# Kernel optimization log

Measured on AMD Instinct MI355X. Metric: run time of the kernel, lower is better.

Reference implementation:

```python
import jax, jax.numpy as jnp
import numpy as np

B, S, N, D = 4, 12, 716, 64
H = 4            # num_heads
ALPHA = 0.2      # LeakyReLU negative slope
NEG = -9e15      # mask fill value from the torch code (-9000000000000000.0)


def setup_inputs() -> dict:
    key = jax.random.key(0)
    ks = jax.random.split(key, 20)
    sc = 1.0 / np.sqrt(D)
    inputs = jax.random.normal(ks[0], (B, S, N, D), dtype=jnp.float32)
    adj = jax.random.randint(ks[1], (N, N), 0, 2).astype(jnp.int32)
    in_degree = jax.random.randint(ks[2], (N,), 0, N)
    out_degree = jax.random.randint(ks[3], (N,), 0, N)
    # embeddings with padding_idx=0 -> row 0 zeroed
    in_emb = (jax.random.normal(ks[4], (N, D)) * sc).at[0].set(0.0)
    out_emb = (jax.random.normal(ks[5], (N, D)) * sc).at[0].set(0.0)
    # GAT params
    W = jax.random.normal(ks[6], (D, D)) * sc
    a1 = jax.random.normal(ks[7], (D, 1)) * sc
    a2 = jax.random.normal(ks[8], (D, 1)) * sc
    # spatial multi-head attention params
    Wq = jax.random.normal(ks[9], (D, D)) * sc
    bq = jnp.zeros((D,))
    Wk = jax.random.normal(ks[10], (D, D)) * sc
    bk = jnp.zeros((D,))
    Wv = jax.random.normal(ks[11], (D, D)) * sc
    bv = jnp.zeros((D,))
    Wo = jax.random.normal(ks[12], (D, D)) * sc
    bo = jnp.zeros((D,))
    # pred_linear: 2D -> D
    Wp = jax.random.normal(ks[13], (2 * D, D)) * (1.0 / np.sqrt(2 * D))
    bp = jnp.zeros((D,))
    return dict(inputs=inputs, adj=adj, in_degree=in_degree, out_degree=out_degree,
                in_emb=in_emb, out_emb=out_emb, W=W, a1=a1, a2=a2,
                Wq=Wq, bq=bq, Wk=Wk, bk=bk, Wv=Wv, bv=bv, Wo=Wo, bo=bo,
                Wp=Wp, bp=bp)


def reference(inputs, adj, in_degree, out_degree, in_emb, out_emb,
              W, a1, a2, Wq, bq, Wk, bk, Wv, bv, Wo, bo, Wp, bp):
    b, s, n, d = inputs.shape
    dh = d // H
    # degree embeddings, broadcast over batch & time: [N, D]
    spatial_emb = in_emb[in_degree] + out_emb[out_degree]

    # ---- GAT, vectorized over all batch*seq samples (orig loops per sample) ----
    x = inputs.reshape(b * s, n, d)
    Wh = jnp.einsum('bnd,de->bne', x, W)                 # [BS, N, D]
    Wh1 = Wh @ a1                                        # [BS, N, 1]
    Wh2 = Wh @ a2                                        # [BS, N, 1]
    e = Wh1 + jnp.swapaxes(Wh2, 1, 2)                    # [BS, N, N]
    e = jnp.where(e > 0, e, ALPHA * e)                   # LeakyReLU
    e = jnp.where(adj[None] > 0, e, NEG)                 # adjacency mask
    attn = jax.nn.softmax(e, axis=-1)                    # softmax(dim=1) on 2D == last axis
    out1 = jax.nn.elu(attn @ Wh).reshape(b, s, n, d)     # dropout is identity in eval

    # ---- Spatial multi-head attention over nodes ----
    y = inputs + spatial_emb                             # [B, S, N, D]
    q = (y @ Wq + bq).reshape(b, s, n, H, dh)
    k = (y @ Wk + bk).reshape(b, s, n, H, dh)
    v = (y @ Wv + bv).reshape(b, s, n, H, dh)
    scores = jnp.einsum('bsnhk,bsmhk->bshnm', q, k) / jnp.sqrt(jnp.float32(dh))
    p = jax.nn.softmax(scores, axis=-1)                  # [B, S, H, N, N]
    o = jnp.einsum('bshnm,bsmhk->bsnhk', p, v).reshape(b, s, n, d)
    out2 = o @ Wo + bo

    # ---- fuse and project ----
    return jnp.concatenate([out1, out2], axis=-1) @ Wp + bp
```

## Files before the change

kernel.cpp:

```cpp
#include <hip/hip_runtime.h>
#include <hip/hip_bf16.h>

#define BN   716
#define BD   64
#define BH   4
#define BDH  16
#define BBS  48
#define NCH  23
#define NJT  45
#define QSCALE 0.3606737602f

typedef __hip_bfloat16 bf16;
typedef __attribute__((ext_vector_type(8))) short short8;
typedef __attribute__((ext_vector_type(4))) short s16x4;
typedef __attribute__((ext_vector_type(4))) float f32x4;

__device__ __forceinline__ float b2f(bf16 x){ return __bfloat162float(x); }
__device__ __forceinline__ bf16 f2b(float x){ return __float2bfloat16(x); }
__device__ __forceinline__ short bfbits(float x){
  union { bf16 h; short s; } c; c.h = __float2bfloat16(x); return c.s;
}
__device__ __forceinline__ unsigned packbf(float a, float b){
  unsigned ua = __float_as_uint(a) + 0x8000u;
  unsigned ub = __float_as_uint(b) + 0x8000u;
  return __builtin_amdgcn_perm(ub, ua, 0x07060302u);
}
__device__ __forceinline__ short8 pack8(float a,float b,float c,float d,
                                        float e,float f,float g,float h){
  short8 r; r[0]=bfbits(a); r[1]=bfbits(b); r[2]=bfbits(c); r[3]=bfbits(d);
  r[4]=bfbits(e); r[5]=bfbits(f); r[6]=bfbits(g); r[7]=bfbits(h); return r;
}
__device__ __forceinline__ float fexp2(float x){
#if __has_builtin(__builtin_amdgcn_exp2f)
  return __builtin_amdgcn_exp2f(x);
#else
  return __expf(x * 0.6931471805599453f);
#endif
}
__device__ __forceinline__ float frcp(float x){
#if __has_builtin(__builtin_amdgcn_rcpf)
  return __builtin_amdgcn_rcpf(x);
#else
  return 1.0f / x;
#endif
}

#define MFMA16(a,b,c) __builtin_amdgcn_mfma_f32_16x16x32_bf16(a,b,c,0,0,0)

#if __has_builtin(__builtin_amdgcn_mfma_f32_16x16x16_bf16)
#define HAVE_MFMA16K 1
__device__ __forceinline__ f32x4 mfma16k(s16x4 a, s16x4 b, f32x4 c){
  return __builtin_amdgcn_mfma_f32_16x16x16_bf16(a, b, c, 0, 0, 0);
}
#elif __has_builtin(__builtin_amdgcn_mfma_f32_16x16x16bf16_1k)
#define HAVE_MFMA16K 1
__device__ __forceinline__ f32x4 mfma16k(s16x4 a, s16x4 b, f32x4 c){
  return __builtin_amdgcn_mfma_f32_16x16x16bf16_1k(a, b, c, 0, 0, 0);
}
#else
#define HAVE_MFMA16K 0
#endif

__global__ __launch_bounds__(256) void k_prep(
    const int* __restrict__ adj,
    const float* __restrict__ W,  const float* __restrict__ Wq,
    const float* __restrict__ Wk, const float* __restrict__ Wv,
    const float* __restrict__ Wo, const float* __restrict__ bo,
    const float* __restrict__ Wp, const float* __restrict__ bp,
    unsigned* __restrict__ mask, bf16* __restrict__ WB,
    bf16* __restrict__ WF, float* __restrict__ bfuse)
{
  int b = blockIdx.x, t = threadIdx.x;
  if (b < 65){
    int w = b * 256 + t;
    if (w < BN * NCH){
      int row = w / NCH, wc = w - row * NCH;
      unsigned m = 0;
      int jb = wc * 32;
      for (int bb = 0; bb < 32; bb++){
        int j = jb + bb;
        if (j < BN && adj[(long)row * BN + j] > 0) m |= (1u << bb);
      }
      mask[w] = m;
    }
  } else if (b < 69){
#pragma unroll
    for (int i = 0; i < 16; i++){
      int idx = (b - 65) * 4096 + i * 256 + t;
      int n = idx >> 6, kk = idx & 63;
      const float* src = (n < 64) ? W : (n < 128) ? Wq : (n < 192) ? Wk : Wv;
      WB[idx] = f2b(src[kk * BD + (n & 63)]);
    }
  } else if (b < 101){
    int idx = (b - 69) * 256 + t;
    int n = idx >> 7, kk = idx & 127;
    float v;
    if (kk < 64){
      v = Wp[kk * BD + n];
    } else {
      v = 0.f;
      int r = kk - 64;
      for (int m = 0; m < BD; m++)
        v += Wo[r * BD + m] * Wp[(BD + m) * BD + n];
    }
    WF[idx] = f2b(v);
  } else {
    if (t < BD){
      float acc = bp[t];
      for (int m = 0; m < BD; m++)
        acc += bo[m] * Wp[(BD + m) * BD + t];
      bfuse[t] = acc;
    }
  }
}

__global__ __launch_bounds__(256) void k_proj(
    const float* __restrict__ x,
    const int* __restrict__ ind, const int* __restrict__ outd,
    const float* __restrict__ in_emb, const float* __restrict__ out_emb,
    const float* __restrict__ a1p, const float* __restrict__ a2p,
    const bf16* __restrict__ WB,
    const float* __restrict__ bq, const float* __restrict__ bk, const float* __restrict__ bv,
    bf16* __restrict__ WhS, float* __restrict__ Wh1, float2* __restrict__ EwP,
    bf16* __restrict__ Qt, bf16* __restrict__ Kt, bf16* __restrict__ Vt16)
{
  __shared__ short stA[64][72];
  __shared__ short stB[64][72];
  __shared__ short stC[64][72];
  __shared__ short stD[64][72];
  int bs = blockIdx.x, tile = blockIdx.y;
  int n0 = tile * 64;
  int t = threadIdx.x, w = t >> 6, lane = t & 63, quad = lane >> 4, l15 = lane & 15;
  long sb = (long)bs * BN;
  int rowi = n0 + w * 16 + l15;
  int rc = rowi < BN ? rowi : BN - 1;
  const float* xr  = x + (sb + rc) * BD;
  const float* ier = in_emb  + (long)ind [rc] * BD;
  const float* oer = out_emb + (long)outd[rc] * BD;

  f32x4 aw[4], aqkv[12];
#pragma unroll
  for (int i2 = 0; i2 < 4;  i2++) aw[i2]   = (f32x4){0,0,0,0};
#pragma unroll
  for (int i2 = 0; i2 < 12; i2++) aqkv[i2] = (f32x4){0,0,0,0};

#pragma unroll
  for (int kc = 0; kc < 2; kc++){
    int k0 = kc * 32 + quad * 8;
    float4 xa = *(const float4*)(xr  + k0);
    float4 xb = *(const float4*)(xr  + k0 + 4);
    float4 ia = *(const float4*)(ier + k0);
    float4 ib = *(const float4*)(ier + k0 + 4);
    float4 oa = *(const float4*)(oer + k0);
    float4 ob = *(const float4*)(oer + k0 + 4);
    short8 ax = pack8(xa.x, xa.y, xa.z, xa.w, xb.x, xb.y, xb.z, xb.w);
    short8 ay = pack8(xa.x+ia.x+oa.x, xa.y+ia.y+oa.y, xa.z+ia.z+oa.z, xa.w+ia.w+oa.w,
                      xb.x+ib.x+ob.x, xb.y+ib.y+ob.y, xb.z+ib.z+ob.z, xb.w+ib.w+ob.w);
#pragma unroll
    for (int nt = 0; nt < 4; nt++)
      aw[nt] = MFMA16(ax, *(const short8*)(WB + (nt*16 + l15) * BD + k0), aw[nt]);
#pragma unroll
    for (int nt = 0; nt < 12; nt++)
      aqkv[nt] = MFMA16(ay, *(const short8*)(WB + (64 + nt*16 + l15) * BD + k0), aqkv[nt]);
  }

  {
    float s1v[4] = {0,0,0,0}, s2v[4] = {0,0,0,0};
#pragma unroll
    for (int nt = 0; nt < 4; nt++){
      float a1f = a1p[nt*16 + l15], a2f = a2p[nt*16 + l15];
#pragma unroll
      for (int reg = 0; reg < 4; reg++){
        s1v[reg] += aw[nt][reg] * a1f;
        s2v[reg] += aw[nt][reg] * a2f;
      }
    }
#pragma unroll
    for (int off = 1; off < 16; off <<= 1){
#pragma unroll
      for (int reg = 0; reg < 4; reg++){
        s1v[reg] += __shfl_xor(s1v[reg], off);
        s2v[reg] += __shfl_xor(s2v[reg], off);
      }
    }
    if (l15 == 0){
#pragma unroll
      for (int reg = 0; reg < 4; reg++){
        int rr = n0 + w*16 + quad*4 + reg;
        if (rr < BN){
          Wh1[sb + rr] = s1v[reg];
          float s2 = s2v[reg];
          EwP[sb + rr] = make_float2(__expf(s2), __expf(0.2f * s2));
        }
      }
    }
  }

#pragma unroll
  for (int nt = 0; nt < 4; nt++){
    *(short4*)&stA[nt*16 + l15][w*16 + quad*4] = make_short4(
        bfbits(aw[nt][0]), bfbits(aw[nt][1]), bfbits(aw[nt][2]), bfbits(aw[nt][3]));
    float bb = bv[nt*16 + l15];
    *(short4*)&stB[nt*16 + l15][w*16 + quad*4] = make_short4(
        bfbits(aqkv[8+nt][0]+bb), bfbits(aqkv[8+nt][1]+bb),
        bfbits(aqkv[8+nt][2]+bb), bfbits(aqkv[8+nt][3]+bb));
    float bq_ = bq[nt*16 + l15];
    float bk_ = bk[nt*16 + l15];
#pragma unroll
    for (int reg = 0; reg < 4; reg++){
      stC[w*16 + quad*4 + reg][nt*16 + l15] = bfbits((aqkv[nt][reg] + bq_) * QSCALE);
      stD[w*16 + quad*4 + reg][nt*16 + l15] = bfbits(aqkv[4+nt][reg] + bk_);
    }
  }
  __syncthreads();

#pragma unroll
  for (int s = 0; s < 2; s++){
    int L = (t*2 + s) * 8;
    int kb = L & 31, d = (L >> 5) & 63, chl = L >> 11;
    int ch = tile * 2 + chl;
    if (ch < NCH)
      *(uint4*)(WhS + (((long)bs*NCH + ch)*64 + d)*32 + kb) = *(const uint4*)&stA[d][chl*32 + kb];
  }
  {
    int jl = t >> 6;
    int c  = t & 15, qq = (t >> 4) & 3;
    int jt = tile * 4 + jl;
    if (jt < NJT){
#pragma unroll
      for (int h = 0; h < BH; h++){
        s16x4 v4 = *(const s16x4*)&stB[h*16 + c][jl*16 + qq*4];
        *(s16x4*)(Vt16 + ((((long)bs*BH + h)*NJT + jt)*64 + (t & 63))*4) = v4;
      }
    }
  }
#pragma unroll
  for (int s = 0; s < 2; s++){
    int L = (t*2 + s) * 8;
    int kb = L & 15, nl = (L >> 4) & 63, h = L >> 10;
    int jt = tile * 4 + (nl >> 4);
    if (jt < NJT){
      *(uint4*)(Qt + ((((long)bs*BH + h)*NJT + jt)*16 + (nl&15))*16 + kb)
          = *(const uint4*)&stC[nl][h*16 + kb];
      *(uint4*)(Kt + ((((long)bs*BH + h)*NJT + jt)*16 + (nl&15))*16 + kb)
          = *(const uint4*)&stD[nl][h*16 + kb];
    }
  }
}

__global__ __launch_bounds__(256) void k_attn(
    const float* __restrict__ Wh1, const float2* __restrict__ EwP,
    const unsigned* __restrict__ mask, const bf16* __restrict__ WhS,
    const bf16* __restrict__ Qt, const bf16* __restrict__ Kt,
    const bf16* __restrict__ Vt16,
    bf16* __restrict__ out1, bf16* __restrict__ o)
{
#if !HAVE_MFMA16K
  __shared__ short pw[4][16][48];
#endif
  int bs = blockIdx.x, yb = blockIdx.y;
  int t = threadIdx.x, w = t >> 6, lane = t & 63, quad = lane >> 4, l15 = lane & 15;
  long sb = (long)bs * BN;

  if (yb < 12){
    int rt = yb * 4 + w;
    if (rt >= NJT) return;
    int i = rt * 16 + l15;
    int ic = i < BN ? i : BN - 1;
    float e1 = Wh1[sb + ic];
    float Aa = __expf(e1), Cc = __expf(0.2f * e1);
    float invA = frcp(Aa);
    const unsigned* mrow = mask + (long)ic * NCH;
    const float2* ew = EwP + sb;

    float sl = 0.f;
    f32x4 acc0 = {0,0,0,0}, acc1 = {0,0,0,0}, acc2 = {0,0,0,0}, acc3 = {0,0,0,0};
    for (int ch = 0; ch < NCH; ch++){
      int j0 = ch * 32 + quad * 8;
      unsigned m8 = (mrow[ch] >> (quad * 8)) & 0xFFu;
      const float4* ef = (const float4*)(ew + j0);
      float4 q0 = ef[0], q1 = ef[1], q2 = ef[2], q3 = ef[3];
      float Bv[8] = {q0.x, q0.z, q1.x, q1.z, q2.x, q2.z, q3.x, q3.z};
      float Dv[8] = {q0.y, q0.w, q1.y, q1.w, q2.y, q2.w, q3.y, q3.w};
      float p[8];
#pragma unroll
      for (int jj = 0; jj < 8; jj++){
        bool cond = Bv[jj] > invA;
        float f = cond ? Bv[jj] : Dv[jj];
        float g = cond ? Aa : Cc;
        float pp = ((m8 >> jj) & 1u) ? f * g : 0.f;
        sl += pp;
        p[jj] = pp;
      }
      union { unsigned u[4]; short8 v; } A;
      A.u[0] = packbf(p[0], p[1]); A.u[1] = packbf(p[2], p[3]);
      A.u[2] = packbf(p[4], p[5]); A.u[3] = packbf(p[6], p[7]);
      const bf16* wbp = WhS + ((long)bs*NCH + ch)*2048 + quad * 8;
      acc0 = MFMA16(A.v, *(const short8*)(wbp + ( 0 + l15) * 32), acc0);
      acc1 = MFMA16(A.v, *(const short8*)(wbp + (16 + l15) * 32), acc1);
      acc2 = MFMA16(A.v, *(const short8*)(wbp + (32 + l15) * 32), acc2);
      acc3 = MFMA16(A.v, *(const short8*)(wbp + (48 + l15) * 32), acc3);
    }
    sl += __shfl_xor(sl, 16);
    sl += __shfl_xor(sl, 32);
    float inv[4];
#pragma unroll
    for (int reg = 0; reg < 4; reg++){
      int srcl = quad * 4 + reg;
      float s = __int_as_float(__builtin_amdgcn_ds_bpermute(srcl << 2, __float_as_int(sl)));
      inv[reg] = 1.0f / s;
    }
    const f32x4* accs[4] = {&acc0, &acc1, &acc2, &acc3};
#pragma unroll
    for (int nt = 0; nt < 4; nt++){
#pragma unroll
      for (int reg = 0; reg < 4; reg++){
        int gi = rt * 16 + quad * 4 + reg;
        if (gi < BN){
          float val = (*accs[nt])[reg] * inv[reg];
          val = (val > 0.f) ? val : (__expf(val) - 1.f);
          out1[(sb + gi) * BD + nt*16 + l15] = f2b(val);
        }
      }
    }
    return;
  }

  int h = w, rt = yb - 12;
  const bf16* Qh = Qt   + ((long)bs*BH + h) * NJT * 256;
  const bf16* Kh = Kt   + ((long)bs*BH + h) * NJT * 256;
  const bf16* Vh = Vt16 + ((long)bs*BH + h) * NJT * 256;

  f32x4 oacc = {0,0,0,0};
  float psum = 0.f;

#if HAVE_MFMA16K
  s16x4 bq16 = *(const s16x4*)(Qh + rt*256 + l15*16 + quad*4);
#pragma unroll 4
  for (int jt = 0; jt < NJT - 1; jt++){
    s16x4 ak = *(const s16x4*)(Kh + jt*256 + l15*16 + quad*4);
    f32x4 c = mfma16k(ak, bq16, ((f32x4){0,0,0,0}));
    float p[4];
#pragma unroll
    for (int reg = 0; reg < 4; reg++){
      float pp = fexp2(c[reg]);
      psum += pp;
      p[reg] = pp;
    }
    union { unsigned u[2]; s16x4 v; } A;
    A.u[0] = packbf(p[0], p[1]); A.u[1] = packbf(p[2], p[3]);
    s16x4 bv = *(const s16x4*)(Vh + jt*256 + lane*4);
    oacc = mfma16k(A.v, bv, oacc);
  }
  {
    int jt = NJT - 1;
    s16x4 ak = *(const s16x4*)(Kh + jt*256 + l15*16 + quad*4);
    f32x4 c = mfma16k(ak, bq16, ((f32x4){0,0,0,0}));
    float p[4];
#pragma unroll
    for (int reg = 0; reg < 4; reg++){
      float pp = (quad == 3) ? 0.f : fexp2(c[reg]);
      psum += pp;
      p[reg] = pp;
    }
    union { unsigned u[2]; s16x4 v; } A;
    A.u[0] = packbf(p[0], p[1]); A.u[1] = packbf(p[2], p[3]);
    s16x4 bv = *(const s16x4*)(Vh + jt*256 + lane*4);
    oacc = mfma16k(A.v, bv, oacc);
  }
#else
  short8 aq = {0,0,0,0,0,0,0,0};
  if (quad < 2) aq = *(const short8*)(Qh + rt*256 + l15*16 + quad*8);
  for (int ch = 0; ch < NCH; ch++){
#pragma unroll
    for (int tt = 0; tt < 2; tt++){
      int jt = 2*ch + tt;
      if (jt < NJT){
        short8 ak = {0,0,0,0,0,0,0,0};
        if (quad < 2) ak = *(const short8*)(Kh + jt*256 + l15*16 + quad*8);
        f32x4 c = MFMA16(ak, aq, ((f32x4){0,0,0,0}));
        bool inval = (jt == NJT-1) && (quad == 3);
#pragma unroll
        for (int reg = 0; reg < 4; reg++){
          float pp = fexp2(c[reg]);
          pp = inval ? 0.f : pp;
          psum += pp;
          pw[h][l15][tt*16 + quad*4 + reg] = (short)((__float_as_uint(pp) + 0x8000u) >> 16);
        }
      } else {
#pragma unroll
        for (int reg = 0; reg < 4; reg++) pw[h][l15][tt*16 + quad*4 + reg] = 0;
      }
    }
    short8 ap = *(const short8*)&pw[h][l15][quad*8];
    int jB = 2*ch + (quad >> 1);
    s16x4 v0 = {0,0,0,0}, v1 = {0,0,0,0};
    if (jB < NJT){
      v0 = *(const s16x4*)(Vh + jB*256 + (((quad&1)*2  )*16 + l15)*4);
      v1 = *(const s16x4*)(Vh + jB*256 + (((quad&1)*2+1)*16 + l15)*4);
    }
    short8 bv8; bv8[0]=v0[0]; bv8[1]=v0[1]; bv8[2]=v0[2]; bv8[3]=v0[3];
    bv8[4]=v1[0]; bv8[5]=v1[1]; bv8[6]=v1[2]; bv8[7]=v1[3];
    oacc = MFMA16(ap, bv8, oacc);
  }
#endif

  psum += __shfl_xor(psum, 16);
  psum += __shfl_xor(psum, 32);
#pragma unroll
  for (int reg = 0; reg < 4; reg++){
    int srcl = quad * 4 + reg;
    float s = __int_as_float(__builtin_amdgcn_ds_bpermute(srcl << 2, __float_as_int(psum)));
    int grow = rt * 16 + srcl;
    if (grow < BN)
      o[(sb + grow) * BD + h * BDH + l15] = f2b(oacc[reg] / s);
  }
}

__global__ __launch_bounds__(256) void k_final(
    const bf16* __restrict__ out1, const bf16* __restrict__ o,
    const bf16* __restrict__ WF, const float* __restrict__ bfuse,
    float* __restrict__ out)
{
  int t = threadIdx.x, w = t >> 6, lane = t & 63, quad = lane >> 4, l15 = lane & 15;
  long r0 = (long)blockIdx.x * 64;
  long row = r0 + w * 16 + l15;
  const bf16* o1r = out1 + row * BD;
  const bf16* oor = o    + row * BD;
  f32x4 acc[4];
#pragma unroll
  for (int i2 = 0; i2 < 4; i2++) acc[i2] = (f32x4){0,0,0,0};
#pragma unroll
  for (int kc = 0; kc < 2; kc++){
    int k0 = kc * 32 + quad * 8;
    short8 a1 = *(const short8*)(o1r + k0);
    short8 a2 = *(const short8*)(oor + k0);
#pragma unroll
    for (int nt = 0; nt < 4; nt++){
      acc[nt] = MFMA16(a1, *(const short8*)(WF + (nt*16 + l15) * 128 + k0), acc[nt]);
      acc[nt] = MFMA16(a2, *(const short8*)(WF + (nt*16 + l15) * 128 + 64 + k0), acc[nt]);
    }
  }
#pragma unroll
  for (int nt = 0; nt < 4; nt++){
    float bf = bfuse[nt*16 + l15];
#pragma unroll
    for (int reg = 0; reg < 4; reg++)
      out[(r0 + w*16 + quad*4 + reg) * BD + nt*16 + l15] = acc[nt][reg] + bf;
  }
}

extern "C" void kernel_launch(void* const* d_in, const int* in_sizes, int n_in,
                              void* d_out, int out_size, void* d_ws, size_t ws_size,
                              hipStream_t stream){
  const float* inp    = (const float*)d_in[0];
  const int*   adj    = (const int*)  d_in[1];
  const int*   ind    = (const int*)  d_in[2];
  const int*   outd   = (const int*)  d_in[3];
  const float* in_emb = (const float*)d_in[4];
  const float* out_emb= (const float*)d_in[5];
  const float* W      = (const float*)d_in[6];
  const float* a1     = (const float*)d_in[7];
  const float* a2     = (const float*)d_in[8];
  const float* Wq     = (const float*)d_in[9];
  const float* bq     = (const float*)d_in[10];
  const float* Wk     = (const float*)d_in[11];
  const float* bk     = (const float*)d_in[12];
  const float* Wv     = (const float*)d_in[13];
  const float* bv     = (const float*)d_in[14];
  const float* Wo     = (const float*)d_in[15];
  const float* bo     = (const float*)d_in[16];
  const float* Wp     = (const float*)d_in[17];
  const float* bp     = (const float*)d_in[18];

  const long PER  = (long)BBS * BN * BD;
  const long WHS  = (long)BBS * NCH * 64 * 32;
  const long QTS  = (long)BBS * BH * NJT * 16 * 16;
  bf16* WhSb  = (bf16*)d_ws;
  bf16* Vt16b = WhSb  + WHS;
  bf16* Qtb   = Vt16b + QTS;
  bf16* Ktb   = Qtb   + QTS;
  bf16* o1B   = Ktb   + QTS;
  bf16* oB    = o1B + PER;
  bf16* WBb   = oB  + PER;
  bf16* WFb   = WBb + 256 * BD;
  unsigned* maskb = (unsigned*)(WFb + BD * 128);
  float2* EwPb = (float2*)(maskb + BN * NCH);
  float* fws  = (float*)(EwPb + (long)BBS * BN + 32);
  float* Wh1  = fws;
  float* bfuse= Wh1 + (long)BBS * BN + 64;

  hipLaunchKernelGGL(k_prep, dim3(102), dim3(256), 0, stream,
                     adj, W, Wq, Wk, Wv, Wo, bo, Wp, bp,
                     maskb, WBb, WFb, bfuse);
  hipLaunchKernelGGL(k_proj, dim3(BBS, 12), dim3(256), 0, stream,
                     inp, ind, outd, in_emb, out_emb, a1, a2, WBb, bq, bk, bv,
                     WhSb, Wh1, EwPb, Qtb, Ktb, Vt16b);
  hipLaunchKernelGGL(k_attn, dim3(BBS, 57), dim3(256), 0, stream,
                     Wh1, EwPb, maskb, WhSb, Qtb, Ktb, Vt16b, o1B, oB);
  hipLaunchKernelGGL(k_final, dim3(537), dim3(256), 0, stream,
                     o1B, oB, WFb, bfuse, (float*)d_out);
}
```

Measured before the change: 180.1 us.

## Pair-interleave K/V tiles for 16-byte loads and shrink attention blocks to two waves

The K and V tiles are stored interleaved in pairs, so the spatial attention loop can fetch two j-tiles per 16-byte load. It then processes them with two independent accumulator chains to expose more MFMA parallelism. The attention kernel drops from 256 to 128 threads per block, and GAT rows and heads are remapped onto a flat per-wave unit index. This removes the idle tail waves of the old 4-wave blocks and balances the load better. The cost is more complex indexing, a special tail tile, and different store patterns in the projection kernel.

```diff
diff --git a/kernel.cpp b/kernel.cpp
--- a/kernel.cpp
+++ b/kernel.cpp
@@ -8,6 +8,9 @@
 #define BBS  48
 #define NCH  23
 #define NJT  45
+#define NJP  22
+#define KVSZ 11520
+#define KVTAIL 11264
 #define QSCALE 0.3606737602f
 
 typedef __hip_bfloat16 bf16;
@@ -122,7 +125,7 @@
     const bf16* __restrict__ WB,
     const float* __restrict__ bq, const float* __restrict__ bk, const float* __restrict__ bv,
     bf16* __restrict__ WhS, float* __restrict__ Wh1, float2* __restrict__ EwP,
-    bf16* __restrict__ Qt, bf16* __restrict__ Kt, bf16* __restrict__ Vt16)
+    bf16* __restrict__ Qt, bf16* __restrict__ Ktp, bf16* __restrict__ Vtp)
 {
   __shared__ short stA[64][72];
   __shared__ short stB[64][72];
@@ -226,11 +229,16 @@
     int jl = t >> 6;
     int c  = t & 15, qq = (t >> 4) & 3;
     int jt = tile * 4 + jl;
+    int L  = t & 63;
     if (jt < NJT){
 #pragma unroll
       for (int h = 0; h < BH; h++){
         s16x4 v4 = *(const s16x4*)&stB[h*16 + c][jl*16 + qq*4];
-        *(s16x4*)(Vt16 + ((((long)bs*BH + h)*NJT + jt)*64 + (t & 63))*4) = v4;
+        long base = ((long)bs*BH + h) * KVSZ;
+        if (jt < 44)
+          *(s16x4*)(Vtp + base + (jt>>1)*512 + L*8 + (jt&1)*4) = v4;
+        else
+          *(s16x4*)(Vtp + base + KVTAIL + L*4) = v4;
       }
     }
   }
@@ -242,29 +250,38 @@
     if (jt < NJT){
       *(uint4*)(Qt + ((((long)bs*BH + h)*NJT + jt)*16 + (nl&15))*16 + kb)
           = *(const uint4*)&stC[nl][h*16 + kb];
-      *(uint4*)(Kt + ((((long)bs*BH + h)*NJT + jt)*16 + (nl&15))*16 + kb)
-          = *(const uint4*)&stD[nl][h*16 + kb];
-    }
-  }
-}
-
-__global__ __launch_bounds__(256) void k_attn(
+      long kbase = ((long)bs*BH + h) * KVSZ;
+      if (jt < 44){
+        s16x4 dlo = *(const s16x4*)&stD[nl][h*16 + kb];
+        s16x4 dhi = *(const s16x4*)&stD[nl][h*16 + kb + 4];
+        long off = kbase + (jt>>1)*512 + (nl&15)*32 + (jt&1)*4;
+        *(s16x4*)(Ktp + off + (kb>>2)*8)     = dlo;
+        *(s16x4*)(Ktp + off + (kb>>2)*8 + 8) = dhi;
+      } else {
+        *(uint4*)(Ktp + kbase + KVTAIL + (nl&15)*16 + kb)
+            = *(const uint4*)&stD[nl][h*16 + kb];
+      }
+    }
+  }
+}
+
+__global__ __launch_bounds__(128) void k_attn(
     const float* __restrict__ Wh1, const float2* __restrict__ EwP,
     const unsigned* __restrict__ mask, const bf16* __restrict__ WhS,
-    const bf16* __restrict__ Qt, const bf16* __restrict__ Kt,
-    const bf16* __restrict__ Vt16,
+    const bf16* __restrict__ Qt, const bf16* __restrict__ Ktp,
+    const bf16* __restrict__ Vtp,
     bf16* __restrict__ out1, bf16* __restrict__ o)
 {
 #if !HAVE_MFMA16K
-  __shared__ short pw[4][16][48];
+  __shared__ short pw[2][16][48];
 #endif
   int bs = blockIdx.x, yb = blockIdx.y;
   int t = threadIdx.x, w = t >> 6, lane = t & 63, quad = lane >> 4, l15 = lane & 15;
+  int unit = yb * 2 + w;
   long sb = (long)bs * BN;
 
-  if (yb < 12){
-    int rt = yb * 4 + w;
-    if (rt >= NJT) return;
+  if (unit < 45){
+    int rt = unit;
     int i = rt * 16 + l15;
     int ic = i < BN ? i : BN - 1;
     float e1 = Wh1[sb + ic];
@@ -325,59 +342,77 @@
     }
     return;
   }
-
-  int h = w, rt = yb - 12;
-  const bf16* Qh = Qt   + ((long)bs*BH + h) * NJT * 256;
-  const bf16* Kh = Kt   + ((long)bs*BH + h) * NJT * 256;
-  const bf16* Vh = Vt16 + ((long)bs*BH + h) * NJT * 256;
-
-  f32x4 oacc = {0,0,0,0};
-  float psum = 0.f;
+  if (unit >= 225) return;
+
+  int u = unit - 45;
+  int h = u / 45, rt = u - h * 45;
+  const bf16* Qh = Qt  + ((long)bs*BH + h) * (long)KVSZ;
+  const bf16* Kh = Ktp + ((long)bs*BH + h) * (long)KVSZ;
+  const bf16* Vh = Vtp + ((long)bs*BH + h) * (long)KVSZ;
 
 #if HAVE_MFMA16K
   s16x4 bq16 = *(const s16x4*)(Qh + rt*256 + l15*16 + quad*4);
-#pragma unroll 4
-  for (int jt = 0; jt < NJT - 1; jt++){
-    s16x4 ak = *(const s16x4*)(Kh + jt*256 + l15*16 + quad*4);
+  f32x4 oA = {0,0,0,0}, oB = {0,0,0,0};
+  float psA = 0.f, psB = 0.f;
+#pragma unroll 2
+  for (int jp = 0; jp < NJP; jp++){
+    short8 akp = *(const short8*)(Kh + jp*512 + l15*32 + quad*8);
+    short8 bvp = *(const short8*)(Vh + jp*512 + lane*8);
+    s16x4 ak0 = {akp[0], akp[1], akp[2], akp[3]};
+    s16x4 ak1 = {akp[4], akp[5], akp[6], akp[7]};
+    f32x4 c0 = mfma16k(ak0, bq16, ((f32x4){0,0,0,0}));
+    f32x4 c1 = mfma16k(ak1, bq16, ((f32x4){0,0,0,0}));
+    float p0[4], p1[4];
+#pragma unroll
+    for (int reg = 0; reg < 4; reg++){
+      float a = fexp2(c0[reg]); psA += a; p0[reg] = a;
+      float b = fexp2(c1[reg]); psB += b; p1[reg] = b;
+    }
+    union { unsigned u2[2]; s16x4 v; } A0, A1;
+    A0.u2[0] = packbf(p0[0], p0[1]); A0.u2[1] = packbf(p0[2], p0[3]);
+    A1.u2[0] = packbf(p1[0], p1[1]); A1.u2[1] = packbf(p1[2], p1[3]);
+    s16x4 bv0 = {bvp[0], bvp[1], bvp[2], bvp[3]};
+    s16x4 bv1 = {bvp[4], bvp[5], bvp[6], bvp[7]};
+    oA = mfma16k(A0.v, bv0, oA);
+    oB = mfma16k(A1.v, bv1, oB);
+  }
+  {
+    s16x4 ak = *(const s16x4*)(Kh + KVTAIL + l15*16 + quad*4);
     f32x4 c = mfma16k(ak, bq16, ((f32x4){0,0,0,0}));
     float p[4];
 #pragma unroll
     for (int reg = 0; reg < 4; reg++){
-      float pp = fexp2(c[reg]);
-      psum += pp;
+      float pp = (quad == 3) ? 0.f : fexp2(c[reg]);
+      psA += pp;
       p[reg] = pp;
     }
-    union { unsigned u[2]; s16x4 v; } A;
-    A.u[0] = packbf(p[0], p[1]); A.u[1] = packbf(p[2], p[3]);
-    s16x4 bv = *(const s16x4*)(Vh + jt*256 + lane*4);
-    oacc = mfma16k(A.v, bv, oacc);
-  }
-  {
-    int jt = NJT - 1;
-    s16x4 ak = *(const s16x4*)(Kh + jt*256 + l15*16 + quad*4);
-    f32x4 c = mfma16k(ak, bq16, ((f32x4){0,0,0,0}));
-    float p[4];
-#pragma unroll
-    for (int reg = 0; reg < 4; reg++){
-      float pp = (quad == 3) ? 0.f : fexp2(c[reg]);
-      psum += pp;
-      p[reg] = pp;
-    }
-    union { unsigned u[2]; s16x4 v; } A;
-    A.u[0] = packbf(p[0], p[1]); A.u[1] = packbf(p[2], p[3]);
-    s16x4 bv = *(const s16x4*)(Vh + jt*256 + lane*4);
-    oacc = mfma16k(A.v, bv, oacc);
-  }
+    union { unsigned u2[2]; s16x4 v; } A;
+    A.u2[0] = packbf(p[0], p[1]); A.u2[1] = packbf(p[2], p[3]);
+    s16x4 bv = *(const s16x4*)(Vh + KVTAIL + lane*4);
+    oA = mfma16k(A.v, bv, oA);
+  }
+  f32x4 oacc = oA + oB;
+  float psum = psA + psB;
 #else
   short8 aq = {0,0,0,0,0,0,0,0};
   if (quad < 2) aq = *(const short8*)(Qh + rt*256 + l15*16 + quad*8);
+  f32x4 oacc = {0,0,0,0};
+  float psum = 0.f;
   for (int ch = 0; ch < NCH; ch++){
 #pragma unroll
     for (int tt = 0; tt < 2; tt++){
       int jt = 2*ch + tt;
       if (jt < NJT){
         short8 ak = {0,0,0,0,0,0,0,0};
-        if (quad < 2) ak = *(const short8*)(Kh + jt*256 + l15*16 + quad*8);
+        if (quad < 2){
+          const bf16* kp = (jt < 44) ? Kh + (jt>>1)*512 + l15*32 + (jt&1)*4
+                                     : Kh + KVTAIL + l15*16;
+          int kstep = (jt < 44) ? 8 : 4;
+          s16x4 klo = *(const s16x4*)(kp + (2*quad)   * kstep);
+          s16x4 khi = *(const s16x4*)(kp + (2*quad+1) * kstep);
+          ak[0]=klo[0]; ak[1]=klo[1]; ak[2]=klo[2]; ak[3]=klo[3];
+          ak[4]=khi[0]; ak[5]=khi[1]; ak[6]=khi[2]; ak[7]=khi[3];
+        }
         f32x4 c = MFMA16(ak, aq, ((f32x4){0,0,0,0}));
         bool inval = (jt == NJT-1) && (quad == 3);
 #pragma unroll
@@ -385,19 +420,23 @@
           float pp = fexp2(c[reg]);
           pp = inval ? 0.f : pp;
           psum += pp;
-          pw[h][l15][tt*16 + quad*4 + reg] = (short)((__float_as_uint(pp) + 0x8000u) >> 16);
+          pw[w][l15][tt*16 + quad*4 + reg] = (short)((__float_as_uint(pp) + 0x8000u) >> 16);
         }
       } else {
 #pragma unroll
-        for (int reg = 0; reg < 4; reg++) pw[h][l15][tt*16 + quad*4 + reg] = 0;
-      }
-    }
-    short8 ap = *(const short8*)&pw[h][l15][quad*8];
+        for (int reg = 0; reg < 4; reg++) pw[w][l15][tt*16 + quad*4 + reg] = 0;
+      }
+    }
+    short8 ap = *(const short8*)&pw[w][l15][quad*8];
     int jB = 2*ch + (quad >> 1);
     s16x4 v0 = {0,0,0,0}, v1 = {0,0,0,0};
     if (jB < NJT){
-      v0 = *(const s16x4*)(Vh + jB*256 + (((quad&1)*2  )*16 + l15)*4);
-      v1 = *(const s16x4*)(Vh + jB*256 + (((quad&1)*2+1)*16 + l15)*4);
+      int L0 = ((quad&1)*2    )*16 + l15;
+      int L1 = ((quad&1)*2 + 1)*16 + l15;
+      const bf16* vp0 = (jB < 44) ? Vh + (jB>>1)*512 + L0*8 + (jB&1)*4 : Vh + KVTAIL + L0*4;
+      const bf16* vp1 = (jB < 44) ? Vh + (jB>>1)*512 + L1*8 + (jB&1)*4 : Vh + KVTAIL + L1*4;
+      v0 = *(const s16x4*)vp0;
+      v1 = *(const s16x4*)vp1;
     }
     short8 bv8; bv8[0]=v0[0]; bv8[1]=v0[1]; bv8[2]=v0[2]; bv8[3]=v0[3];
     bv8[4]=v1[0]; bv8[5]=v1[1]; bv8[6]=v1[2]; bv8[7]=v1[3];
@@ -475,12 +514,12 @@
 
   const long PER  = (long)BBS * BN * BD;
   const long WHS  = (long)BBS * NCH * 64 * 32;
-  const long QTS  = (long)BBS * BH * NJT * 16 * 16;
+  const long QTS  = (long)BBS * BH * KVSZ;
   bf16* WhSb  = (bf16*)d_ws;
-  bf16* Vt16b = WhSb  + WHS;
-  bf16* Qtb   = Vt16b + QTS;
-  bf16* Ktb   = Qtb   + QTS;
-  bf16* o1B   = Ktb   + QTS;
+  bf16* Vtpb  = WhSb + WHS;
+  bf16* Qtb   = Vtpb + QTS;
+  bf16* Ktpb  = Qtb  + QTS;
+  bf16* o1B   = Ktpb + QTS;
   bf16* oB    = o1B + PER;
   bf16* WBb   = oB  + PER;
   bf16* WFb   = WBb + 256 * BD;
@@ -495,9 +534,9 @@
                      maskb, WBb, WFb, bfuse);
   hipLaunchKernelGGL(k_proj, dim3(BBS, 12), dim3(256), 0, stream,
                      inp, ind, outd, in_emb, out_emb, a1, a2, WBb, bq, bk, bv,
-                     WhSb, Wh1, EwPb, Qtb, Ktb, Vt16b);
-  hipLaunchKernelGGL(k_attn, dim3(BBS, 57), dim3(256), 0, stream,
-                     Wh1, EwPb, maskb, WhSb, Qtb, Ktb, Vt16b, o1B, oB);
+                     WhSb, Wh1, EwPb, Qtb, Ktpb, Vtpb);
+  hipLaunchKernelGGL(k_attn, dim3(BBS, 113), dim3(128), 0, stream,
+                     Wh1, EwPb, maskb, WhSb, Qtb, Ktpb, Vtpb, o1B, oB);
   hipLaunchKernelGGL(k_final, dim3(537), dim3(256), 0, stream,
                      o1B, oB, WFb, bfuse, (float*)d_out);
 }
```

Result: faster. 173.6 us (-3.6%).
